# Performance work log

Measured on AMD Instinct MI355X. Metric: run time of the kernel, lower is better.

## Reference

```python
import jax, jax.numpy as jnp
import numpy as np

DIM = 2048
HID = 5632
ZERO_POINT = 128.0


def _qlinear(x, wq, scale):
    # wq: uint8-style codes stored as int32, shape [out, in]; scale: [out]
    W = (wq.astype(jnp.float32) - ZERO_POINT) * scale[:, None]  # dequant [out, in]
    return jnp.einsum('bsd,hd->bsh', x, W)


def setup_inputs() -> dict:
    key = jax.random.key(0)
    ks = jax.random.split(key, 7)
    B, S = 4, 2048
    # scale chosen so dequantized weights have ~1/sqrt(fan_in) magnitude
    sg = jax.random.uniform(ks[1], (HID,)) * (0.02 / np.sqrt(DIM)) + 1e-4
    su = jax.random.uniform(ks[3], (HID,)) * (0.02 / np.sqrt(DIM)) + 1e-4
    sd = jax.random.uniform(ks[5], (DIM,)) * (0.02 / np.sqrt(HID)) + 1e-4
    return {
        'x': jax.random.normal(ks[0], (B, S, DIM), dtype=jnp.float32),
        'wq_gate': jax.random.randint(ks[2], (HID, DIM), 0, 256, dtype=jnp.int32),
        's_gate': sg,
        'wq_up': jax.random.randint(ks[4], (HID, DIM), 0, 256, dtype=jnp.int32),
        's_up': su,
        'wq_down': jax.random.randint(ks[6], (DIM, HID), 0, 256, dtype=jnp.int32),
        's_down': sd,
    }


def reference(x, wq_gate, s_gate, wq_up, s_up, wq_down, s_down):
    gate = _qlinear(x, wq_gate, s_gate)          # [B, S, HID]
    gate = jax.nn.silu(gate)
    up = _qlinear(x, wq_up, s_up)                # [B, S, HID]
    return _qlinear(gate * up, wq_down, s_down)  # [B, S, DIM]
```

## Files before the change

### kernel.cpp

```cpp
#include <hip/hip_runtime.h>
#include <hip/hip_bf16.h>
#include <stdint.h>

#define DIM 2048
#define HID 5632
#define BM 128
#define BN 128
#define BK 32

typedef __attribute__((ext_vector_type(8))) short short8;
typedef __attribute__((ext_vector_type(4))) float f32x4;
typedef __attribute__((ext_vector_type(4))) int int4v;
typedef __attribute__((ext_vector_type(4))) unsigned short ushort4v;

__device__ __forceinline__ unsigned short f32_to_bf16_rne(float f) {
    union { float f; unsigned u; } v; v.f = f;
    unsigned u = v.u;
    return (unsigned short)((u + 0x7FFFu + ((u >> 16) & 1u)) >> 16);
}

__device__ __forceinline__ void gload16(const void* g, void* l) {
    __builtin_amdgcn_global_load_lds(
        (const __attribute__((address_space(1))) void*)g,
        (__attribute__((address_space(3))) void*)l,
        16, 0, 0);
}

__global__ void dequant_bf16(const int* __restrict__ wq, const float* __restrict__ scale,
                             unsigned short* __restrict__ out, long total, int cols) {
    long n4 = total >> 2;
    long stride = (long)gridDim.x * blockDim.x;
    for (long i = (long)blockIdx.x * blockDim.x + threadIdx.x; i < n4; i += stride) {
        int4v c = ((const int4v*)wq)[i];
        int row = (int)((i << 2) / cols);
        float s = scale[row];
        ushort4v o;
        o.x = f32_to_bf16_rne(((float)c.x - 128.0f) * s);
        o.y = f32_to_bf16_rne(((float)c.y - 128.0f) * s);
        o.z = f32_to_bf16_rne(((float)c.z - 128.0f) * s);
        o.w = f32_to_bf16_rne(((float)c.w - 128.0f) * s);
        ((ushort4v*)out)[i] = o;
    }
}

__global__ void cast_f32_bf16(const float* __restrict__ in, unsigned short* __restrict__ out, long n) {
    long n4 = n >> 2;
    long stride = (long)gridDim.x * blockDim.x;
    for (long i = (long)blockIdx.x * blockDim.x + threadIdx.x; i < n4; i += stride) {
        f32x4 v = ((const f32x4*)in)[i];
        ushort4v o;
        o.x = f32_to_bf16_rne(v[0]);
        o.y = f32_to_bf16_rne(v[1]);
        o.z = f32_to_bf16_rne(v[2]);
        o.w = f32_to_bf16_rne(v[3]);
        ((ushort4v*)out)[i] = o;
    }
}

__global__ __launch_bounds__(256, 2) void gemm_gateup(
    const unsigned short* __restrict__ X,
    const unsigned short* __restrict__ Wg,
    const unsigned short* __restrict__ Wu,
    unsigned short* __restrict__ H, int M)
{
    __shared__ __attribute__((aligned(16))) unsigned short As[BM * BK];
    __shared__ __attribute__((aligned(16))) unsigned short Bgs[BN * BK];
    __shared__ __attribute__((aligned(16))) unsigned short Bus[BN * BK];

    const int tid  = threadIdx.x;
    const int lane = tid & 63;
    const int wid  = tid >> 6;
    const int wr   = wid >> 1, wc = wid & 1;
    const int m0 = blockIdx.x * BM;
    const int n0 = blockIdx.y * BN;

    const int idx0 = tid, idx1 = tid + 256;
    const int r0 = idx0 >> 2, c0 = (idx0 & 3) << 3;
    const int r1 = idx1 >> 2, c1 = (idx1 & 3) << 3;

    const unsigned short* A0 = X  + (size_t)(m0 + r0) * DIM + c0;
    const unsigned short* A1 = X  + (size_t)(m0 + r1) * DIM + c1;
    const unsigned short* G0 = Wg + (size_t)(n0 + r0) * DIM + c0;
    const unsigned short* G1 = Wg + (size_t)(n0 + r1) * DIM + c1;
    const unsigned short* U0 = Wu + (size_t)(n0 + r0) * DIM + c0;
    const unsigned short* U1 = Wu + (size_t)(n0 + r1) * DIM + c1;

    f32x4 accg[4][4] = {};
    f32x4 accu[4][4] = {};

    const int lr = lane & 15;
    const int kr = (lane >> 4) << 3;

    for (int k0 = 0; k0 < DIM; k0 += BK) {
        gload16(A0 + k0, &As[idx0 * 8]);
        gload16(A1 + k0, &As[idx1 * 8]);
        gload16(G0 + k0, &Bgs[idx0 * 8]);
        gload16(G1 + k0, &Bgs[idx1 * 8]);
        gload16(U0 + k0, &Bus[idx0 * 8]);
        gload16(U1 + k0, &Bus[idx1 * 8]);
        __syncthreads();

        short8 a[4], bg[4], bu[4];
        #pragma unroll
        for (int i = 0; i < 4; ++i)
            a[i] = *(const short8*)&As[(wr * 64 + i * 16 + lr) * BK + kr];
        #pragma unroll
        for (int i = 0; i < 4; ++i)
            bg[i] = *(const short8*)&Bgs[(wc * 64 + i * 16 + lr) * BK + kr];
        #pragma unroll
        for (int i = 0; i < 4; ++i)
            bu[i] = *(const short8*)&Bus[(wc * 64 + i * 16 + lr) * BK + kr];

        #pragma unroll
        for (int i = 0; i < 4; ++i) {
            #pragma unroll
            for (int j = 0; j < 4; ++j) {
                accg[i][j] = __builtin_amdgcn_mfma_f32_16x16x32_bf16(a[i], bg[j], accg[i][j], 0, 0, 0);
                accu[i][j] = __builtin_amdgcn_mfma_f32_16x16x32_bf16(a[i], bu[j], accu[i][j], 0, 0, 0);
            }
        }
        __syncthreads();
    }

    const int lg = lane >> 4;
    #pragma unroll
    for (int i = 0; i < 4; ++i) {
        #pragma unroll
        for (int j = 0; j < 4; ++j) {
            #pragma unroll
            for (int e = 0; e < 4; ++e) {
                int row = m0 + wr * 64 + i * 16 + lg * 4 + e;
                int col = n0 + wc * 64 + j * 16 + lr;
                float g = accg[i][j][e];
                float u = accu[i][j][e];
                float sg = g / (1.0f + __expf(-g));
                H[(size_t)row * HID + col] = f32_to_bf16_rne(sg * u);
            }
        }
    }
}

__global__ __launch_bounds__(256, 2) void gemm_down(
    const unsigned short* __restrict__ Hb,
    const unsigned short* __restrict__ Wd,
    float* __restrict__ Out, int M)
{
    __shared__ __attribute__((aligned(16))) unsigned short As[BM * BK];
    __shared__ __attribute__((aligned(16))) unsigned short Bs[BN * BK];

    const int tid  = threadIdx.x;
    const int lane = tid & 63;
    const int wid  = tid >> 6;
    const int wr   = wid >> 1, wc = wid & 1;
    const int m0 = blockIdx.x * BM;
    const int n0 = blockIdx.y * BN;

    const int idx0 = tid, idx1 = tid + 256;
    const int r0 = idx0 >> 2, c0 = (idx0 & 3) << 3;
    const int r1 = idx1 >> 2, c1 = (idx1 & 3) << 3;

    const unsigned short* A0 = Hb + (size_t)(m0 + r0) * HID + c0;
    const unsigned short* A1 = Hb + (size_t)(m0 + r1) * HID + c1;
    const unsigned short* B0 = Wd + (size_t)(n0 + r0) * HID + c0;
    const unsigned short* B1 = Wd + (size_t)(n0 + r1) * HID + c1;

    f32x4 acc[4][4] = {};

    const int lr = lane & 15;
    const int kr = (lane >> 4) << 3;

    for (int k0 = 0; k0 < HID; k0 += BK) {
        gload16(A0 + k0, &As[idx0 * 8]);
        gload16(A1 + k0, &As[idx1 * 8]);
        gload16(B0 + k0, &Bs[idx0 * 8]);
        gload16(B1 + k0, &Bs[idx1 * 8]);
        __syncthreads();

        short8 a[4], b[4];
        #pragma unroll
        for (int i = 0; i < 4; ++i)
            a[i] = *(const short8*)&As[(wr * 64 + i * 16 + lr) * BK + kr];
        #pragma unroll
        for (int i = 0; i < 4; ++i)
            b[i] = *(const short8*)&Bs[(wc * 64 + i * 16 + lr) * BK + kr];

        #pragma unroll
        for (int i = 0; i < 4; ++i) {
            #pragma unroll
            for (int j = 0; j < 4; ++j) {
                acc[i][j] = __builtin_amdgcn_mfma_f32_16x16x32_bf16(a[i], b[j], acc[i][j], 0, 0, 0);
            }
        }
        __syncthreads();
    }

    const int lg = lane >> 4;
    #pragma unroll
    for (int i = 0; i < 4; ++i) {
        #pragma unroll
        for (int j = 0; j < 4; ++j) {
            #pragma unroll
            for (int e = 0; e < 4; ++e) {
                int row = m0 + wr * 64 + i * 16 + lg * 4 + e;
                int col = n0 + wc * 64 + j * 16 + lr;
                Out[(size_t)row * DIM + col] = acc[i][j][e];
            }
        }
    }
}

extern "C" void kernel_launch(void* const* d_in, const int* in_sizes, int n_in,
                              void* d_out, int out_size, void* d_ws, size_t ws_size,
                              hipStream_t stream) {
    const float* x      = (const float*)d_in[0];
    const int* wq_gate  = (const int*)d_in[1];
    const float* s_gate = (const float*)d_in[2];
    const int* wq_up    = (const int*)d_in[3];
    const float* s_up   = (const float*)d_in[4];
    const int* wq_down  = (const int*)d_in[5];
    const float* s_down = (const float*)d_in[6];
    float* out = (float*)d_out;

    const int M = in_sizes[0] / DIM;

    char* ws = (char*)d_ws;
    unsigned short* xb = (unsigned short*)ws;
    unsigned short* w1 = (unsigned short*)(ws + (size_t)M * DIM * 2);
    unsigned short* w2 = w1 + (size_t)HID * DIM;
    unsigned short* h  = w2 + (size_t)HID * DIM;

    cast_f32_bf16<<<2048, 256, 0, stream>>>(x, xb, (long)M * DIM);
    dequant_bf16<<<2048, 256, 0, stream>>>(wq_gate, s_gate, w1, (long)HID * DIM, DIM);
    dequant_bf16<<<2048, 256, 0, stream>>>(wq_up, s_up, w2, (long)HID * DIM, DIM);

    gemm_gateup<<<dim3(M / BM, HID / BN), 256, 0, stream>>>(xb, w1, w2, h, M);

    dequant_bf16<<<2048, 256, 0, stream>>>(wq_down, s_down, w1, (long)DIM * HID, HID);

    gemm_down<<<dim3(M / BM, DIM / BN), 256, 0, stream>>>(h, w1, out, M);
}
```

Baseline: 692.9 us.

## Interleave gate/up weights and use 256x256 double-buffered swizzled GEMM tiles

Dequantization now writes gate and up weights into one interleaved matrix, with rows alternating in 16-row groups. That lets a single GEMM compute both projections, with gate and up accumulators side by side in registers. Both GEMMs move to 256x256x64 tiles on 512 threads, use double-buffered LDS with an XOR swizzle against bank conflicts, overlap loads with compute via explicit vmcnt waits, and raise wave priority around the MFMA blocks. The aim is higher arithmetic intensity and hidden global-load latency. The cost is 128KB of LDS per block and heavy register pressure, so occupancy will be lower.

```diff
diff --git a/kernel.cpp b/kernel.cpp
--- a/kernel.cpp
+++ b/kernel.cpp
@@ -4,9 +4,6 @@
 
 #define DIM 2048
 #define HID 5632
-#define BM 128
-#define BN 128
-#define BK 32
 
 typedef __attribute__((ext_vector_type(8))) short short8;
 typedef __attribute__((ext_vector_type(4))) float f32x4;
@@ -26,8 +23,8 @@
         16, 0, 0);
 }
 
-__global__ void dequant_bf16(const int* __restrict__ wq, const float* __restrict__ scale,
-                             unsigned short* __restrict__ out, long total, int cols) {
+__global__ void dequant_plain(const int* __restrict__ wq, const float* __restrict__ scale,
+                              unsigned short* __restrict__ out, long total, int cols) {
     long n4 = total >> 2;
     long stride = (long)gridDim.x * blockDim.x;
     for (long i = (long)blockIdx.x * blockDim.x + threadIdx.x; i < n4; i += stride) {
@@ -43,6 +40,32 @@
     }
 }
 
+__global__ void dequant_gateup(const int* __restrict__ wg, const float* __restrict__ sg,
+                               const int* __restrict__ wu, const float* __restrict__ su,
+                               unsigned short* __restrict__ out) {
+    const long n4 = (long)HID * DIM / 4;
+    long stride = (long)gridDim.x * blockDim.x;
+    for (long i = (long)blockIdx.x * blockDim.x + threadIdx.x; i < n4; i += stride) {
+        int r  = (int)(i >> 9);
+        int c4 = (int)(i & 511);
+        int rp = ((r >> 4) << 5) + (r & 15);
+        float s1 = sg[r], s2 = su[r];
+        int4v g = ((const int4v*)wg)[i];
+        int4v u = ((const int4v*)wu)[i];
+        ushort4v og, ou;
+        og.x = f32_to_bf16_rne(((float)g.x - 128.0f) * s1);
+        og.y = f32_to_bf16_rne(((float)g.y - 128.0f) * s1);
+        og.z = f32_to_bf16_rne(((float)g.z - 128.0f) * s1);
+        og.w = f32_to_bf16_rne(((float)g.w - 128.0f) * s1);
+        ou.x = f32_to_bf16_rne(((float)u.x - 128.0f) * s2);
+        ou.y = f32_to_bf16_rne(((float)u.y - 128.0f) * s2);
+        ou.z = f32_to_bf16_rne(((float)u.z - 128.0f) * s2);
+        ou.w = f32_to_bf16_rne(((float)u.w - 128.0f) * s2);
+        ((ushort4v*)out)[(long)rp * 512 + c4]        = og;
+        ((ushort4v*)out)[(long)(rp + 16) * 512 + c4] = ou;
+    }
+}
+
 __global__ void cast_f32_bf16(const float* __restrict__ in, unsigned short* __restrict__ out, long n) {
     long n4 = n >> 2;
     long stride = (long)gridDim.x * blockDim.x;
@@ -57,153 +80,229 @@
     }
 }
 
-__global__ __launch_bounds__(256, 2) void gemm_gateup(
+
+__global__ __launch_bounds__(512, 2) void gemm_gateup(
     const unsigned short* __restrict__ X,
-    const unsigned short* __restrict__ Wg,
-    const unsigned short* __restrict__ Wu,
-    unsigned short* __restrict__ H, int M)
+    const unsigned short* __restrict__ Wp,
+    unsigned short* __restrict__ H)
 {
-    __shared__ __attribute__((aligned(16))) unsigned short As[BM * BK];
-    __shared__ __attribute__((aligned(16))) unsigned short Bgs[BN * BK];
-    __shared__ __attribute__((aligned(16))) unsigned short Bus[BN * BK];
+    __shared__ __attribute__((aligned(16))) unsigned short As[2][256 * 64];
+    __shared__ __attribute__((aligned(16))) unsigned short Bs[2][256 * 64];
 
     const int tid  = threadIdx.x;
     const int lane = tid & 63;
     const int wid  = tid >> 6;
-    const int wr   = wid >> 1, wc = wid & 1;
-    const int m0 = blockIdx.x * BM;
-    const int n0 = blockIdx.y * BN;
-
-    const int idx0 = tid, idx1 = tid + 256;
-    const int r0 = idx0 >> 2, c0 = (idx0 & 3) << 3;
-    const int r1 = idx1 >> 2, c1 = (idx1 & 3) << 3;
-
-    const unsigned short* A0 = X  + (size_t)(m0 + r0) * DIM + c0;
-    const unsigned short* A1 = X  + (size_t)(m0 + r1) * DIM + c1;
-    const unsigned short* G0 = Wg + (size_t)(n0 + r0) * DIM + c0;
-    const unsigned short* G1 = Wg + (size_t)(n0 + r1) * DIM + c1;
-    const unsigned short* U0 = Wu + (size_t)(n0 + r0) * DIM + c0;
-    const unsigned short* U1 = Wu + (size_t)(n0 + r1) * DIM + c1;
-
-    f32x4 accg[4][4] = {};
-    f32x4 accu[4][4] = {};
-
-    const int lr = lane & 15;
-    const int kr = (lane >> 4) << 3;
-
-    for (int k0 = 0; k0 < DIM; k0 += BK) {
-        gload16(A0 + k0, &As[idx0 * 8]);
-        gload16(A1 + k0, &As[idx1 * 8]);
-        gload16(G0 + k0, &Bgs[idx0 * 8]);
-        gload16(G1 + k0, &Bgs[idx1 * 8]);
-        gload16(U0 + k0, &Bus[idx0 * 8]);
-        gload16(U1 + k0, &Bus[idx1 * 8]);
-        __syncthreads();
-
-        short8 a[4], bg[4], bu[4];
-        #pragma unroll
-        for (int i = 0; i < 4; ++i)
-            a[i] = *(const short8*)&As[(wr * 64 + i * 16 + lr) * BK + kr];
-        #pragma unroll
-        for (int i = 0; i < 4; ++i)
-            bg[i] = *(const short8*)&Bgs[(wc * 64 + i * 16 + lr) * BK + kr];
-        #pragma unroll
-        for (int i = 0; i < 4; ++i)
-            bu[i] = *(const short8*)&Bus[(wc * 64 + i * 16 + lr) * BK + kr];
-
-        #pragma unroll
-        for (int i = 0; i < 4; ++i) {
-            #pragma unroll
-            for (int j = 0; j < 4; ++j) {
-                accg[i][j] = __builtin_amdgcn_mfma_f32_16x16x32_bf16(a[i], bg[j], accg[i][j], 0, 0, 0);
-                accu[i][j] = __builtin_amdgcn_mfma_f32_16x16x32_bf16(a[i], bu[j], accu[i][j], 0, 0, 0);
+    const int wr   = wid >> 2;
+    const int wc   = wid & 3;
+    const int m0   = blockIdx.x << 8;
+    const int n0   = blockIdx.y << 8;
+    const int lr   = lane & 15;
+    const int kg   = lane >> 4;
+
+    int srow[4], skc[4], sdst[4];
+    #pragma unroll
+    for (int l = 0; l < 4; ++l) {
+        int q = l * 512 + tid;
+        srow[l] = q >> 3;
+        skc[l]  = (((q & 7) ^ ((q >> 3) & 7)) << 3);
+        sdst[l] = q << 3;
+    }
+
+    auto STAGE = [&](int buf, int kt) {
+        const int kk = kt << 6;
+        #pragma unroll
+        for (int l = 0; l < 4; ++l) {
+            gload16(X  + (size_t)(m0 + srow[l]) * DIM + kk + skc[l], &As[buf][sdst[l]]);
+            gload16(Wp + (size_t)(n0 + srow[l]) * DIM + kk + skc[l], &Bs[buf][sdst[l]]);
+        }
+    };
+
+    f32x4 acc[8][4];
+    #pragma unroll
+    for (int m = 0; m < 8; ++m)
+        #pragma unroll
+        for (int n = 0; n < 4; ++n) acc[m][n] = (f32x4){0.f, 0.f, 0.f, 0.f};
+
+    const int c0 = ((kg ^ (lr & 7)) << 3);
+    const int c1 = (((4 + kg) ^ (lr & 7)) << 3);
+    const int abase = (wr * 128 + lr) * 64;
+    const int bbase = (wc * 64 + lr) * 64;
+
+    STAGE(0, 0);
+    STAGE(1, 1);
+
+    const int NT = DIM / 64;
+    for (int kt = 0; kt < NT; ++kt) {
+        const int cur = kt & 1;
+        if (kt < NT - 1) asm volatile("s_waitcnt vmcnt(8)" ::: "memory");
+        else             asm volatile("s_waitcnt vmcnt(0)" ::: "memory");
+        __builtin_amdgcn_s_barrier();
+        __builtin_amdgcn_sched_barrier(0);
+
+        const unsigned short* ap0 = &As[cur][abase + c0];
+        const unsigned short* ap1 = &As[cur][abase + c1];
+        const unsigned short* bp0 = &Bs[cur][bbase + c0];
+        const unsigned short* bp1 = &Bs[cur][bbase + c1];
+
+        short8 a0[8], a1[8], b0[4], b1[4];
+        #pragma unroll
+        for (int n = 0; n < 4; ++n) {
+            b0[n] = *(const short8*)(bp0 + (n << 10));
+            b1[n] = *(const short8*)(bp1 + (n << 10));
+        }
+        #pragma unroll
+        for (int m = 0; m < 8; ++m) {
+            a0[m] = *(const short8*)(ap0 + (m << 10));
+            a1[m] = *(const short8*)(ap1 + (m << 10));
+        }
+
+        __builtin_amdgcn_s_setprio(1);
+        #pragma unroll
+        for (int m = 0; m < 8; ++m)
+            #pragma unroll
+            for (int n = 0; n < 4; ++n)
+                acc[m][n] = __builtin_amdgcn_mfma_f32_16x16x32_bf16(a0[m], b0[n], acc[m][n], 0, 0, 0);
+        __builtin_amdgcn_s_setprio(0);
+        __builtin_amdgcn_s_setprio(1);
+        #pragma unroll
+        for (int m = 0; m < 8; ++m)
+            #pragma unroll
+            for (int n = 0; n < 4; ++n)
+                acc[m][n] = __builtin_amdgcn_mfma_f32_16x16x32_bf16(a1[m], b1[n], acc[m][n], 0, 0, 0);
+        __builtin_amdgcn_s_setprio(0);
+
+        __builtin_amdgcn_sched_barrier(0);
+        __builtin_amdgcn_s_barrier();
+        __builtin_amdgcn_sched_barrier(0);
+        if (kt + 2 < NT) STAGE(cur, kt + 2);
+        __builtin_amdgcn_sched_barrier(0);
+    }
+
+    const int lg = lane >> 4;
+    #pragma unroll
+    for (int m = 0; m < 8; ++m) {
+        #pragma unroll
+        for (int i = 0; i < 2; ++i) {
+            f32x4 g = acc[m][2 * i], u = acc[m][2 * i + 1];
+            const int col = (blockIdx.y << 7) + wc * 32 + i * 16 + lr;
+            #pragma unroll
+            for (int e = 0; e < 4; ++e) {
+                const int row = m0 + wr * 128 + m * 16 + lg * 4 + e;
+                float gv = g[e];
+                float sg = gv / (1.0f + __expf(-gv));
+                H[(size_t)row * HID + col] = f32_to_bf16_rne(sg * u[e]);
             }
         }
-        __syncthreads();
-    }
-
-    const int lg = lane >> 4;
-    #pragma unroll
-    for (int i = 0; i < 4; ++i) {
-        #pragma unroll
-        for (int j = 0; j < 4; ++j) {
-            #pragma unroll
-            for (int e = 0; e < 4; ++e) {
-                int row = m0 + wr * 64 + i * 16 + lg * 4 + e;
-                int col = n0 + wc * 64 + j * 16 + lr;
-                float g = accg[i][j][e];
-                float u = accu[i][j][e];
-                float sg = g / (1.0f + __expf(-g));
-                H[(size_t)row * HID + col] = f32_to_bf16_rne(sg * u);
-            }
-        }
-    }
-}
-
-__global__ __launch_bounds__(256, 2) void gemm_down(
+    }
+}
+
+__global__ __launch_bounds__(512, 2) void gemm_down(
     const unsigned short* __restrict__ Hb,
     const unsigned short* __restrict__ Wd,
-    float* __restrict__ Out, int M)
+    float* __restrict__ Out)
 {
-    __shared__ __attribute__((aligned(16))) unsigned short As[BM * BK];
-    __shared__ __attribute__((aligned(16))) unsigned short Bs[BN * BK];
+    __shared__ __attribute__((aligned(16))) unsigned short As[2][256 * 64];
+    __shared__ __attribute__((aligned(16))) unsigned short Bs[2][256 * 64];
 
     const int tid  = threadIdx.x;
     const int lane = tid & 63;
     const int wid  = tid >> 6;
-    const int wr   = wid >> 1, wc = wid & 1;
-    const int m0 = blockIdx.x * BM;
-    const int n0 = blockIdx.y * BN;
-
-    const int idx0 = tid, idx1 = tid + 256;
-    const int r0 = idx0 >> 2, c0 = (idx0 & 3) << 3;
-    const int r1 = idx1 >> 2, c1 = (idx1 & 3) << 3;
-
-    const unsigned short* A0 = Hb + (size_t)(m0 + r0) * HID + c0;
-    const unsigned short* A1 = Hb + (size_t)(m0 + r1) * HID + c1;
-    const unsigned short* B0 = Wd + (size_t)(n0 + r0) * HID + c0;
-    const unsigned short* B1 = Wd + (size_t)(n0 + r1) * HID + c1;
-
-    f32x4 acc[4][4] = {};
-
-    const int lr = lane & 15;
-    const int kr = (lane >> 4) << 3;
-
-    for (int k0 = 0; k0 < HID; k0 += BK) {
-        gload16(A0 + k0, &As[idx0 * 8]);
-        gload16(A1 + k0, &As[idx1 * 8]);
-        gload16(B0 + k0, &Bs[idx0 * 8]);
-        gload16(B1 + k0, &Bs[idx1 * 8]);
-        __syncthreads();
-
-        short8 a[4], b[4];
-        #pragma unroll
-        for (int i = 0; i < 4; ++i)
-            a[i] = *(const short8*)&As[(wr * 64 + i * 16 + lr) * BK + kr];
-        #pragma unroll
-        for (int i = 0; i < 4; ++i)
-            b[i] = *(const short8*)&Bs[(wc * 64 + i * 16 + lr) * BK + kr];
-
-        #pragma unroll
-        for (int i = 0; i < 4; ++i) {
-            #pragma unroll
-            for (int j = 0; j < 4; ++j) {
-                acc[i][j] = __builtin_amdgcn_mfma_f32_16x16x32_bf16(a[i], b[j], acc[i][j], 0, 0, 0);
-            }
-        }
-        __syncthreads();
+    const int wr   = wid >> 2;
+    const int wc   = wid & 3;
+    const int m0   = blockIdx.x << 8;
+    const int n0   = blockIdx.y << 8;
+    const int lr   = lane & 15;
+    const int kg   = lane >> 4;
+
+    int srow[4], skc[4], sdst[4];
+    #pragma unroll
+    for (int l = 0; l < 4; ++l) {
+        int q = l * 512 + tid;
+        srow[l] = q >> 3;
+        skc[l]  = (((q & 7) ^ ((q >> 3) & 7)) << 3);
+        sdst[l] = q << 3;
+    }
+
+    auto STAGE = [&](int buf, int kt) {
+        const int kk = kt << 6;
+        #pragma unroll
+        for (int l = 0; l < 4; ++l) {
+            gload16(Hb + (size_t)(m0 + srow[l]) * HID + kk + skc[l], &As[buf][sdst[l]]);
+            gload16(Wd + (size_t)(n0 + srow[l]) * HID + kk + skc[l], &Bs[buf][sdst[l]]);
+        }
+    };
+
+    f32x4 acc[8][4];
+    #pragma unroll
+    for (int m = 0; m < 8; ++m)
+        #pragma unroll
+        for (int n = 0; n < 4; ++n) acc[m][n] = (f32x4){0.f, 0.f, 0.f, 0.f};
+
+    const int c0 = ((kg ^ (lr & 7)) << 3);
+    const int c1 = (((4 + kg) ^ (lr & 7)) << 3);
+    const int abase = (wr * 128 + lr) * 64;
+    const int bbase = (wc * 64 + lr) * 64;
+
+    STAGE(0, 0);
+    STAGE(1, 1);
+
+    const int NT = HID / 64;
+    for (int kt = 0; kt < NT; ++kt) {
+        const int cur = kt & 1;
+        if (kt < NT - 1) asm volatile("s_waitcnt vmcnt(8)" ::: "memory");
+        else             asm volatile("s_waitcnt vmcnt(0)" ::: "memory");
+        __builtin_amdgcn_s_barrier();
+        __builtin_amdgcn_sched_barrier(0);
+
+        const unsigned short* ap0 = &As[cur][abase + c0];
+        const unsigned short* ap1 = &As[cur][abase + c1];
+        const unsigned short* bp0 = &Bs[cur][bbase + c0];
+        const unsigned short* bp1 = &Bs[cur][bbase + c1];
+
+        short8 a0[8], a1[8], b0[4], b1[4];
+        #pragma unroll
+        for (int n = 0; n < 4; ++n) {
+            b0[n] = *(const short8*)(bp0 + (n << 10));
+            b1[n] = *(const short8*)(bp1 + (n << 10));
+        }
+        #pragma unroll
+        for (int m = 0; m < 8; ++m) {
+            a0[m] = *(const short8*)(ap0 + (m << 10));
+            a1[m] = *(const short8*)(ap1 + (m << 10));
+        }
+
+        __builtin_amdgcn_s_setprio(1);
+        #pragma unroll
+        for (int m = 0; m < 8; ++m)
+            #pragma unroll
+            for (int n = 0; n < 4; ++n)
+                acc[m][n] = __builtin_amdgcn_mfma_f32_16x16x32_bf16(a0[m], b0[n], acc[m][n], 0, 0, 0);
+        __builtin_amdgcn_s_setprio(0);
+        __builtin_amdgcn_s_setprio(1);
+        #pragma unroll
+        for (int m = 0; m < 8; ++m)
+            #pragma unroll
+            for (int n = 0; n < 4; ++n)
+                acc[m][n] = __builtin_amdgcn_mfma_f32_16x16x32_bf16(a1[m], b1[n], acc[m][n], 0, 0, 0);
+        __builtin_amdgcn_s_setprio(0);
+
+        __builtin_amdgcn_sched_barrier(0);
+        __builtin_amdgcn_s_barrier();
+        __builtin_amdgcn_sched_barrier(0);
+        if (kt + 2 < NT) STAGE(cur, kt + 2);
+        __builtin_amdgcn_sched_barrier(0);
     }
 
     const int lg = lane >> 4;
     #pragma unroll
-    for (int i = 0; i < 4; ++i) {
-        #pragma unroll
-        for (int j = 0; j < 4; ++j) {
+    for (int m = 0; m < 8; ++m) {
+        #pragma unroll
+        for (int n = 0; n < 4; ++n) {
+            const int col = n0 + wc * 64 + n * 16 + lr;
             #pragma unroll
             for (int e = 0; e < 4; ++e) {
-                int row = m0 + wr * 64 + i * 16 + lg * 4 + e;
-                int col = n0 + wc * 64 + j * 16 + lr;
-                Out[(size_t)row * DIM + col] = acc[i][j][e];
+                const int row = m0 + wr * 128 + m * 16 + lg * 4 + e;
+                Out[(size_t)row * DIM + col] = acc[m][n][e];
             }
         }
     }
@@ -223,19 +322,16 @@
 
     const int M = in_sizes[0] / DIM;
 
-    char* ws = (char*)d_ws;
-    unsigned short* xb = (unsigned short*)ws;
-    unsigned short* w1 = (unsigned short*)(ws + (size_t)M * DIM * 2);
-    unsigned short* w2 = w1 + (size_t)HID * DIM;
-    unsigned short* h  = w2 + (size_t)HID * DIM;
+    unsigned short* xb  = (unsigned short*)d_ws;
+    unsigned short* wgu = xb + (size_t)M * DIM;
+    unsigned short* h   = wgu + (size_t)2 * HID * DIM;
 
     cast_f32_bf16<<<2048, 256, 0, stream>>>(x, xb, (long)M * DIM);
-    dequant_bf16<<<2048, 256, 0, stream>>>(wq_gate, s_gate, w1, (long)HID * DIM, DIM);
-    dequant_bf16<<<2048, 256, 0, stream>>>(wq_up, s_up, w2, (long)HID * DIM, DIM);
-
-    gemm_gateup<<<dim3(M / BM, HID / BN), 256, 0, stream>>>(xb, w1, w2, h, M);
-
-    dequant_bf16<<<2048, 256, 0, stream>>>(wq_down, s_down, w1, (long)DIM * HID, HID);
-
-    gemm_down<<<dim3(M / BM, DIM / BN), 256, 0, stream>>>(h, w1, out, M);
-}
+    dequant_gateup<<<2048, 256, 0, stream>>>(wq_gate, s_gate, wq_up, s_up, wgu);
+
+    gemm_gateup<<<dim3(M / 256, (2 * HID) / 256), 512, 0, stream>>>(xb, wgu, h);
+
+    dequant_plain<<<2048, 256, 0, stream>>>(wq_down, s_down, wgu, (long)DIM * HID, HID);
+
+    gemm_down<<<dim3(M / 256, DIM / 256), 512, 0, stream>>>(h, wgu, out);
+}
```

Result: faster. 587.7 us (-15.2%).
